# Optimization experiments

Hardware: AMD Instinct MI355X
Metric: run time of the kernel (lower is better)

The kernel has to match this reference:

```python
import jax, jax.numpy as jnp
import numpy as np

B, S, W, D, T = 64, 512, 384, 768, 21


def setup_inputs() -> dict:
    key = jax.random.key(0)
    ks = jax.random.split(key, 8)
    hidden_states = jax.random.normal(ks[0], (B, S, D), dtype=jnp.float32)  # BERT last_hidden_state
    word_maps = jnp.sort(jax.random.randint(ks[1], (B, W), 0, S), axis=1)  # first-subword index per word
    tags = jax.random.randint(ks[2], (B, W), 0, T)
    word_mask = jnp.ones((B, W), dtype=bool)  # torchcrf requires mask[:,0] all on
    W_tag = jax.random.normal(ks[3], (T, D), dtype=jnp.float32) * 0.02  # hidden2tag weight
    b_tag = jnp.zeros((T,), dtype=jnp.float32)
    start_trans = jax.random.uniform(ks[4], (T,), minval=-0.1, maxval=0.1)
    end_trans = jax.random.uniform(ks[5], (T,), minval=-0.1, maxval=0.1)
    trans = jax.random.uniform(ks[6], (T, T), minval=-0.1, maxval=0.1)
    return dict(hidden_states=hidden_states, W_tag=W_tag, b_tag=b_tag,
                start_trans=start_trans, end_trans=end_trans, trans=trans,
                word_maps=word_maps, tags=tags, word_mask=word_mask)


def reference(hidden_states, W_tag, b_tag, start_trans, end_trans, trans,
              word_maps, tags, word_mask):
    # --- ragged subword -> word gather (vectorized form of the python loop) ---
    word_feats = jnp.take_along_axis(hidden_states, word_maps[:, :, None], axis=1)  # [B,W,D]
    # dropout is identity in eval / deterministic reference
    emissions = jnp.einsum('bwd,td->bwt', word_feats, W_tag) + b_tag  # [B,W,T]

    maskf = word_mask.astype(emissions.dtype)
    bidx = jnp.arange(tags.shape[0])

    # --- CRF numerator: score of the given tag sequence ---
    emit_sc = jnp.take_along_axis(emissions, tags[:, :, None], axis=2)[..., 0]  # [B,W]
    trans_sc = trans[tags[:, :-1], tags[:, 1:]]                                  # [B,W-1]
    num = start_trans[tags[:, 0]] + emit_sc[:, 0]
    num = num + jnp.sum((trans_sc + emit_sc[:, 1:]) * maskf[:, 1:], axis=1)
    lengths = word_mask.sum(axis=1)
    last_tags = jnp.take_along_axis(tags, (lengths - 1)[:, None], axis=1)[:, 0]
    num = num + end_trans[last_tags]

    # --- CRF denominator: log partition via forward recurrence (scan over time) ---
    def step(score, xm):
        em_t, m_t = xm  # [B,T], [B]
        nxt = jax.nn.logsumexp(score[:, :, None] + trans[None, :, :] + em_t[:, None, :], axis=1)
        return jnp.where(m_t[:, None], nxt, score), None

    score0 = start_trans[None, :] + emissions[:, 0]  # [B,T]
    score, _ = jax.lax.scan(step, score0,
                            (jnp.swapaxes(emissions[:, 1:], 0, 1), word_mask[:, 1:].T))
    log_z = jax.nn.logsumexp(score + end_trans[None, :], axis=1)  # [B]

    llh = num - log_z
    return -jnp.mean(llh)  # reduction='mean', negated
```

## Files before the change

kernel.cpp:

```cpp
#include <hip/hip_runtime.h>
#include <math.h>

#define BB 64
#define SS 512
#define WW 384
#define DD 768
#define TT 21
#define ROWS (BB*WW)
#define EMSTRIDE (WW*TT)
#define NCH 16
#define CLEN 24
#define PSTRIDE 24
#define PMATSZ (TT*PSTRIDE)
#define LN32 3.4657359027997265f

typedef short   bf16x8 __attribute__((ext_vector_type(8)));
typedef float   f32x4  __attribute__((ext_vector_type(4)));
union FragU { bf16x8 v; unsigned u[4]; };

__device__ __forceinline__ unsigned pack_bf16(unsigned lo, unsigned hi) {
    return __builtin_amdgcn_perm(hi, lo, 0x07060302);
}

__global__ __launch_bounds__(256) void emissions_kernel(
    const float* __restrict__ hidden, const int* __restrict__ word_maps,
    const float* __restrict__ W_tag, const float* __restrict__ b_tag,
    float* __restrict__ em, float* __restrict__ out)
{
    __shared__ __align__(16) unsigned short Bs[24 * 2 * 4 * 16 * 8];
    __shared__ __align__(16) float Sred[2][64][8];
    __shared__ int rowoff[32];

    const int tid = threadIdx.x;
    const int rowBase = blockIdx.x * 32;

    if (blockIdx.x == 0 && tid == 0) out[0] = 0.0f;

    if (tid < 32) {
        int row = rowBase + tid;
        int b = row / WW;
        int w = row - b * WW;
        rowoff[tid] = b * SS + word_maps[b * WW + w];
    }

    for (int i = tid; i < TT * (DD / 4); i += 256) {
        int t = i / (DD / 4), q = i - t * (DD / 4);
        int k  = q * 4;
        int ks = k >> 5, quad = (k >> 3) & 3, e = k & 7;
        int nt = t >> 4, l16 = t & 15;
        float4 wv = *(const float4*)&W_tag[t * DD + k];
        int off = ((ks * 2 + nt) * 4 + quad) * 128 + l16 * 8 + e;
        *(unsigned*)&Bs[off]     = pack_bf16(__float_as_uint(wv.x), __float_as_uint(wv.y));
        *(unsigned*)&Bs[off + 2] = pack_bf16(__float_as_uint(wv.z), __float_as_uint(wv.w));
    }
    __syncthreads();

    const int wv_  = tid >> 6;
    const int rt   = wv_ >> 1;
    const int h    = wv_ & 1;
    const int lane = tid & 63;
    const int l16  = lane & 15;
    const int quad = lane >> 4;

    const float* abase = hidden + (size_t)rowoff[rt * 16 + l16] * DD
                                + h * (DD / 2) + quad * 8;
    const unsigned short* bbase = Bs + quad * 128 + l16 * 8 + h * 12 * 1024;

    f32x4 acc0 = {}, acc1 = {};

    float4 A0[4], A1[4];
    #pragma unroll
    for (int p = 0; p < 4; ++p) {
        A0[p] = *(const float4*)(abase + p * 32);
        A1[p] = *(const float4*)(abase + p * 32 + 4);
    }
    bf16x8 b0c = *(const bf16x8*)(bbase);
    bf16x8 b1c = *(const bf16x8*)(bbase + 512);

    #pragma unroll
    for (int ks = 0; ks < 12; ++ks) {
        bf16x8 b0n = b0c, b1n = b1c;
        if (ks < 11) {
            b0n = *(const bf16x8*)(bbase + (ks + 1) * 1024);
            b1n = *(const bf16x8*)(bbase + (ks + 1) * 1024 + 512);
        }
        FragU a;
        a.u[0] = pack_bf16(__float_as_uint(A0[ks & 3].x), __float_as_uint(A0[ks & 3].y));
        a.u[1] = pack_bf16(__float_as_uint(A0[ks & 3].z), __float_as_uint(A0[ks & 3].w));
        a.u[2] = pack_bf16(__float_as_uint(A1[ks & 3].x), __float_as_uint(A1[ks & 3].y));
        a.u[3] = pack_bf16(__float_as_uint(A1[ks & 3].z), __float_as_uint(A1[ks & 3].w));
        if (ks < 8) {
            A0[ks & 3] = *(const float4*)(abase + (ks + 4) * 32);
            A1[ks & 3] = *(const float4*)(abase + (ks + 4) * 32 + 4);
        }
        acc0 = __builtin_amdgcn_mfma_f32_16x16x32_bf16(a.v, b0c, acc0, 0, 0, 0);
        acc1 = __builtin_amdgcn_mfma_f32_16x16x32_bf16(a.v, b1c, acc1, 0, 0, 0);
        b0c = b0n; b1c = b1n;
    }

    if (h == 1) {
        #pragma unroll
        for (int r = 0; r < 4; ++r) {
            Sred[rt][lane][r]     = acc0[r];
            Sred[rt][lane][r + 4] = acc1[r];
        }
    }
    __syncthreads();

    if (h == 0) {
        #pragma unroll
        for (int r = 0; r < 4; ++r) {
            acc0[r] += Sred[rt][lane][r];
            acc1[r] += Sred[rt][lane][r + 4];
        }
        int rbase = rowBase + rt * 16 + quad * 4;
        {
            float bt = b_tag[l16];
            #pragma unroll
            for (int r = 0; r < 4; ++r)
                em[(size_t)(rbase + r) * TT + l16] = acc0[r] + bt;
        }
        if (16 + l16 < TT) {
            float bt = b_tag[16 + l16];
            #pragma unroll
            for (int r = 0; r < 4; ++r)
                em[(size_t)(rbase + r) * TT + 16 + l16] = acc1[r] + bt;
        }
    }
}

__global__ __launch_bounds__(256, 1) void chunk_kernel(
    const float* __restrict__ em, const float* __restrict__ trans,
    float* __restrict__ Pmat)
{
    __shared__ __align__(16) float Pbuf[4][2][PMATSZ];
    __shared__ __align__(16) float gem[4][CLEN * PSTRIDE];

    const int wid  = threadIdx.x >> 6;
    const int lane = threadIdx.x & 63;
    const int id   = blockIdx.x * 4 + wid;
    const int b    = id >> 4;
    const int c    = id & (NCH - 1);
    const int s0   = 1 + c * CLEN;
    const int n    = (c == NCH - 1) ? (WW - s0) : CLEN;

    int i3r = lane / 6;
    const int jg  = lane - i3r * 6;
    const bool active = (i3r < 7) && (jg < 6);
    const int i3 = (i3r < 7) ? i3r : 6;
    const int jbase = (jg < 6 ? jg : 5) * 4;

    float4 etr[CLEN];
    #pragma unroll
    for (int k = 0; k < CLEN; ++k) {
        float4 e = make_float4(0.f, 0.f, 0.f, 0.f);
        if (k < TT) {
            e.x = (jbase + 0 < TT) ? __expf(trans[k * TT + jbase + 0]) * 0.03125f : 0.f;
            e.y = (jbase + 1 < TT) ? __expf(trans[k * TT + jbase + 1]) * 0.03125f : 0.f;
            e.z = (jbase + 2 < TT) ? __expf(trans[k * TT + jbase + 2]) * 0.03125f : 0.f;
            e.w = (jbase + 3 < TT) ? __expf(trans[k * TT + jbase + 3]) * 0.03125f : 0.f;
        }
        etr[k] = e;
    }

    for (int idx = lane; idx < n * PSTRIDE; idx += 64) {
        int tt = idx / PSTRIDE, j = idx - tt * PSTRIDE;
        float g = 1.0f;
        if (j < TT) g = __expf(em[((size_t)b * WW + (s0 + tt)) * TT + j]);
        gem[wid][idx] = g;
    }

    {
        float4 g = *(const float4*)&gem[wid][0 * PSTRIDE + jbase];
        #pragma unroll
        for (int r = 0; r < 3; ++r) {
            int i = i3 * 3 + r;
            float4 e = etr[i];
            float4 v = make_float4(e.x * g.x, e.y * g.y, e.z * g.z, e.w * g.w);
            if (active) *(float4*)&Pbuf[wid][0][i * PSTRIDE + jbase] = v;
        }
    }
    __syncthreads();

    int pp = 0;
    for (int tt = 1; tt < n; ++tt) {
        float acc[3][4];
        #pragma unroll
        for (int r = 0; r < 3; ++r)
            #pragma unroll
            for (int q = 0; q < 4; ++q) acc[r][q] = 0.f;

        const float* Pc = &Pbuf[wid][pp][0];
        #pragma unroll
        for (int kb = 0; kb < 6; ++kb) {
            float4 p0 = *(const float4*)&Pc[(i3 * 3 + 0) * PSTRIDE + kb * 4];
            float4 p1 = *(const float4*)&Pc[(i3 * 3 + 1) * PSTRIDE + kb * 4];
            float4 p2 = *(const float4*)&Pc[(i3 * 3 + 2) * PSTRIDE + kb * 4];
            #pragma unroll
            for (int kk = 0; kk < 4; ++kk) {
                float4 e = etr[kb * 4 + kk];
                float a = (kk == 0) ? p0.x : (kk == 1) ? p0.y : (kk == 2) ? p0.z : p0.w;
                float bv= (kk == 0) ? p1.x : (kk == 1) ? p1.y : (kk == 2) ? p1.z : p1.w;
                float cv= (kk == 0) ? p2.x : (kk == 1) ? p2.y : (kk == 2) ? p2.z : p2.w;
                acc[0][0] = fmaf(a, e.x, acc[0][0]); acc[0][1] = fmaf(a, e.y, acc[0][1]);
                acc[0][2] = fmaf(a, e.z, acc[0][2]); acc[0][3] = fmaf(a, e.w, acc[0][3]);
                acc[1][0] = fmaf(bv, e.x, acc[1][0]); acc[1][1] = fmaf(bv, e.y, acc[1][1]);
                acc[1][2] = fmaf(bv, e.z, acc[1][2]); acc[1][3] = fmaf(bv, e.w, acc[1][3]);
                acc[2][0] = fmaf(cv, e.x, acc[2][0]); acc[2][1] = fmaf(cv, e.y, acc[2][1]);
                acc[2][2] = fmaf(cv, e.z, acc[2][2]); acc[2][3] = fmaf(cv, e.w, acc[2][3]);
            }
        }
        float4 g = *(const float4*)&gem[wid][tt * PSTRIDE + jbase];
        if (active) {
            #pragma unroll
            for (int r = 0; r < 3; ++r) {
                float4 v = make_float4(acc[r][0] * g.x, acc[r][1] * g.y,
                                       acc[r][2] * g.z, acc[r][3] * g.w);
                *(float4*)&Pbuf[wid][1 - pp][(i3 * 3 + r) * PSTRIDE + jbase] = v;
            }
        }
        pp ^= 1;
    }

    float* dst = Pmat + (size_t)id * PMATSZ;
    for (int idx = lane; idx < PMATSZ; idx += 64)
        dst[idx] = Pbuf[wid][pp][idx];
}

__device__ __forceinline__ float lane_bcast(float v, int l) {
    return __uint_as_float(__builtin_amdgcn_readlane(__float_as_uint(v), l));
}

__global__ __launch_bounds__(64, 1) void combine_kernel(
    const float* __restrict__ Pmat, const float* __restrict__ em,
    const int* __restrict__ tags, const float* __restrict__ start_trans,
    const float* __restrict__ end_trans, const float* __restrict__ trans,
    float* __restrict__ out)
{
    const int b = blockIdx.x;
    const int j = threadIdx.x;
    const bool act = (j < TT);
    const int jc = act ? j : (TT - 1);
    const float* emb = em + (size_t)b * EMSTRIDE;

    float s0v = start_trans[jc] + emb[jc];
    float M = act ? s0v : -1e30f;
    #pragma unroll
    for (int o = 32; o > 0; o >>= 1) M = fmaxf(M, __shfl_xor(M, o));
    float sig = act ? __expf(s0v - M) : 0.0f;

    for (int c = 0; c < NCH; ++c) {
        const float* P = Pmat + (size_t)(b * NCH + c) * PMATSZ;
        float col[TT];
        #pragma unroll
        for (int i = 0; i < TT; ++i) col[i] = P[i * PSTRIDE + jc];
        float a0 = 0.f, a1 = 0.f, a2 = 0.f;
        #pragma unroll
        for (int i = 0; i < TT; i += 3) {
            a0 = fmaf(lane_bcast(sig, i    ), col[i    ], a0);
            a1 = fmaf(lane_bcast(sig, i + 1), col[i + 1], a1);
            a2 = fmaf(lane_bcast(sig, i + 2), col[i + 2], a2);
        }
        float v = act ? (a0 + a1 + a2) : 0.0f;
        float m = v;
        #pragma unroll
        for (int o = 32; o > 0; o >>= 1) m = fmaxf(m, __shfl_xor(m, o));
        int nst = (c == NCH - 1) ? (WW - (1 + c * CLEN)) : CLEN;
        M += __logf(m) + (float)nst * LN32;
        sig = v / m;
    }

    float fin = (act && sig > 0.f) ? (M + __logf(sig) + end_trans[jc]) : -1e30f;
    float mm = fin;
    #pragma unroll
    for (int o = 32; o > 0; o >>= 1) mm = fmaxf(mm, __shfl_xor(mm, o));
    float pe = __expf(fin - mm);
    float ssum = pe;
    #pragma unroll
    for (int o = 32; o > 0; o >>= 1) ssum += __shfl_xor(ssum, o);
    float lz = mm + __logf(ssum);

    const int* tb = tags + b * WW;
    float part = 0.f;
    for (int w = j; w < WW; w += 64) {
        int tw = tb[w];
        float e = emb[w * TT + tw];
        float tsc = (w == 0) ? start_trans[tw] : trans[tb[w - 1] * TT + tw];
        part += tsc + e;
    }
    #pragma unroll
    for (int o = 32; o > 0; o >>= 1) part += __shfl_xor(part, o);

    if (j == 0) {
        float num = part + end_trans[tb[WW - 1]];
        atomicAdd(out, -(num - lz) * (1.0f / BB));
    }
}

extern "C" void kernel_launch(void* const* d_in, const int* in_sizes, int n_in,
                              void* d_out, int out_size, void* d_ws, size_t ws_size,
                              hipStream_t stream) {
    const float* hidden      = (const float*)d_in[0];
    const float* W_tag       = (const float*)d_in[1];
    const float* b_tag       = (const float*)d_in[2];
    const float* start_trans = (const float*)d_in[3];
    const float* end_trans   = (const float*)d_in[4];
    const float* trans       = (const float*)d_in[5];
    const int*   word_maps   = (const int*)  d_in[6];
    const int*   tags        = (const int*)  d_in[7];

    float* out  = (float*)d_out;
    float* em   = (float*)d_ws;
    float* Pmat = (float*)d_ws + (size_t)ROWS * TT;

    emissions_kernel<<<ROWS / 32, 256, 0, stream>>>(hidden, word_maps, W_tag, b_tag, em, out);
    chunk_kernel<<<BB * NCH / 4, 256, 0, stream>>>(em, trans, Pmat);
    combine_kernel<<<BB, 64, 0, stream>>>(Pmat, em, tags, start_trans, end_trans, trans, out);
}
```

Before: 209.2 us.

## Move exp(trans) table to shared memory and store chunk matrices transposed

The chunk kernel stops holding the scaled exp(trans) table in 96 registers per lane. It builds the table once per block in shared memory and reads float4s from LDS inside the recurrence, which should cut register pressure at the cost of extra LDS traffic. The chunk product matrices are now written transposed, padded to 24x24, so the combine kernel can load each column with contiguous float4 reads instead of 21 strided scalar loads. Pmat grows slightly, and the barrier moves to after the table and gem fill.

```diff
diff --git a/kernel.cpp b/kernel.cpp
--- a/kernel.cpp
+++ b/kernel.cpp
@@ -12,6 +12,7 @@
 #define CLEN 24
 #define PSTRIDE 24
 #define PMATSZ (TT*PSTRIDE)
+#define PTSZ (PSTRIDE*PSTRIDE)
 #define LN32 3.4657359027997265f
 
 typedef short   bf16x8 __attribute__((ext_vector_type(8)));
@@ -133,54 +134,48 @@
     const float* __restrict__ em, const float* __restrict__ trans,
     float* __restrict__ Pmat)
 {
+    __shared__ __align__(16) float Es[PTSZ];
     __shared__ __align__(16) float Pbuf[4][2][PMATSZ];
     __shared__ __align__(16) float gem[4][CLEN * PSTRIDE];
 
-    const int wid  = threadIdx.x >> 6;
-    const int lane = threadIdx.x & 63;
+    const int tid  = threadIdx.x;
+    const int wid  = tid >> 6;
+    const int lane = tid & 63;
     const int id   = blockIdx.x * 4 + wid;
     const int b    = id >> 4;
     const int c    = id & (NCH - 1);
     const int s0   = 1 + c * CLEN;
     const int n    = (c == NCH - 1) ? (WW - s0) : CLEN;
 
+    for (int idx = tid; idx < PTSZ; idx += 256) {
+        int k = idx / PSTRIDE, j = idx - k * PSTRIDE;
+        Es[idx] = (k < TT && j < TT) ? __expf(trans[k * TT + j]) * 0.03125f : 0.f;
+    }
+
     int i3r = lane / 6;
     const int jg  = lane - i3r * 6;
     const bool active = (i3r < 7) && (jg < 6);
     const int i3 = (i3r < 7) ? i3r : 6;
     const int jbase = (jg < 6 ? jg : 5) * 4;
 
-    float4 etr[CLEN];
-    #pragma unroll
-    for (int k = 0; k < CLEN; ++k) {
-        float4 e = make_float4(0.f, 0.f, 0.f, 0.f);
-        if (k < TT) {
-            e.x = (jbase + 0 < TT) ? __expf(trans[k * TT + jbase + 0]) * 0.03125f : 0.f;
-            e.y = (jbase + 1 < TT) ? __expf(trans[k * TT + jbase + 1]) * 0.03125f : 0.f;
-            e.z = (jbase + 2 < TT) ? __expf(trans[k * TT + jbase + 2]) * 0.03125f : 0.f;
-            e.w = (jbase + 3 < TT) ? __expf(trans[k * TT + jbase + 3]) * 0.03125f : 0.f;
-        }
-        etr[k] = e;
-    }
-
     for (int idx = lane; idx < n * PSTRIDE; idx += 64) {
         int tt = idx / PSTRIDE, j = idx - tt * PSTRIDE;
         float g = 1.0f;
         if (j < TT) g = __expf(em[((size_t)b * WW + (s0 + tt)) * TT + j]);
         gem[wid][idx] = g;
     }
+    __syncthreads();
 
     {
-        float4 g = *(const float4*)&gem[wid][0 * PSTRIDE + jbase];
+        float4 g = *(const float4*)&gem[wid][jbase];
         #pragma unroll
         for (int r = 0; r < 3; ++r) {
             int i = i3 * 3 + r;
-            float4 e = etr[i];
+            float4 e = *(const float4*)&Es[i * PSTRIDE + jbase];
             float4 v = make_float4(e.x * g.x, e.y * g.y, e.z * g.z, e.w * g.w);
             if (active) *(float4*)&Pbuf[wid][0][i * PSTRIDE + jbase] = v;
         }
     }
-    __syncthreads();
 
     int pp = 0;
     for (int tt = 1; tt < n; ++tt) {
@@ -198,7 +193,8 @@
             float4 p2 = *(const float4*)&Pc[(i3 * 3 + 2) * PSTRIDE + kb * 4];
             #pragma unroll
             for (int kk = 0; kk < 4; ++kk) {
-                float4 e = etr[kb * 4 + kk];
+                const int k = kb * 4 + kk;
+                float4 e = *(const float4*)&Es[k * PSTRIDE + jbase];
                 float a = (kk == 0) ? p0.x : (kk == 1) ? p0.y : (kk == 2) ? p0.z : p0.w;
                 float bv= (kk == 0) ? p1.x : (kk == 1) ? p1.y : (kk == 2) ? p1.z : p1.w;
                 float cv= (kk == 0) ? p2.x : (kk == 1) ? p2.y : (kk == 2) ? p2.z : p2.w;
@@ -222,9 +218,12 @@
         pp ^= 1;
     }
 
-    float* dst = Pmat + (size_t)id * PMATSZ;
-    for (int idx = lane; idx < PMATSZ; idx += 64)
-        dst[idx] = Pbuf[wid][pp][idx];
+    float* dst = Pmat + (size_t)id * PTSZ;
+    const float* Pf = &Pbuf[wid][pp][0];
+    for (int idx = lane; idx < PTSZ; idx += 64) {
+        int j = idx / PSTRIDE, i = idx - j * PSTRIDE;
+        dst[idx] = (i < TT) ? Pf[i * PSTRIDE + j] : 0.f;
+    }
 }
 
 __device__ __forceinline__ float lane_bcast(float v, int l) {
@@ -250,10 +249,20 @@
     float sig = act ? __expf(s0v - M) : 0.0f;
 
     for (int c = 0; c < NCH; ++c) {
-        const float* P = Pmat + (size_t)(b * NCH + c) * PMATSZ;
+        const float* PT = Pmat + (size_t)(b * NCH + c) * PTSZ + jc * PSTRIDE;
+        float4 c0 = *(const float4*)&PT[0];
+        float4 c1 = *(const float4*)&PT[4];
+        float4 c2 = *(const float4*)&PT[8];
+        float4 c3 = *(const float4*)&PT[12];
+        float4 c4 = *(const float4*)&PT[16];
+        float  c5 = PT[20];
         float col[TT];
-        #pragma unroll
-        for (int i = 0; i < TT; ++i) col[i] = P[i * PSTRIDE + jc];
+        col[0]=c0.x;  col[1]=c0.y;  col[2]=c0.z;  col[3]=c0.w;
+        col[4]=c1.x;  col[5]=c1.y;  col[6]=c1.z;  col[7]=c1.w;
+        col[8]=c2.x;  col[9]=c2.y;  col[10]=c2.z; col[11]=c2.w;
+        col[12]=c3.x; col[13]=c3.y; col[14]=c3.z; col[15]=c3.w;
+        col[16]=c4.x; col[17]=c4.y; col[18]=c4.z; col[19]=c4.w;
+        col[20]=c5;
         float a0 = 0.f, a1 = 0.f, a2 = 0.f;
         #pragma unroll
         for (int i = 0; i < TT; i += 3) {
```

After: 195.3 us. 6.6% less time.
